# Kernel optimization log

Hardware: AMD Instinct MI355X
Metric: run time of the kernel (lower is better)

The kernel has to match this reference:

```python
import jax, jax.numpy as jnp
import numpy as np

P = 16
D = 768          # latent_dim
H = 3072         # hidden_dim
B = 256
OUT_DIMS = [100 + 10 * i for i in range(P)]   # sum = 2800
MAX_OUT = max(OUT_DIMS)
EPS = 1e-5


def setup_inputs() -> dict:
    key = jax.random.key(0)
    ks = jax.random.split(key, 6)
    x = jax.random.normal(ks[0], (B, P, D), dtype=jnp.float32)
    # LayerNorm params per part (torch default init: gamma=1, beta=0)
    gamma = jnp.ones((P, D), dtype=jnp.float32)
    beta = jnp.zeros((P, D), dtype=jnp.float32)
    # fc1: Linear(D, H, bias=False) per part -> stacked [P, H, D]
    w1 = jax.random.normal(ks[1], (P, H, D), dtype=jnp.float32) * 0.02
    # fc2: Linear(H, out_dims[i], bias=True) per part, padded to MAX_OUT.
    # Padded rows are never read (sliced away at concat).
    w2 = jax.random.normal(ks[2], (P, MAX_OUT, H), dtype=jnp.float32) * 0.02
    b2 = jnp.zeros((P, MAX_OUT), dtype=jnp.float32)
    return {"x": x, "gamma": gamma, "beta": beta, "w1": w1, "w2": w2, "b2": b2}


def reference(x, gamma, beta, w1, w2, b2):
    # Per-part LayerNorm over latent dim (torch uses biased variance)
    mu = jnp.mean(x, axis=-1, keepdims=True)
    var = jnp.mean(jnp.square(x - mu), axis=-1, keepdims=True)
    xn = (x - mu) * jax.lax.rsqrt(var + EPS) * gamma[None] + beta[None]  # [B,P,D]
    # fc1 (no bias) + exact GELU (torch.nn.GELU default)
    h = jnp.einsum('bpd,phd->bph', xn, w1)          # [B,P,H]
    h = jax.nn.gelu(h, approximate=False)
    # dropout p=0.0 -> identity
    # fc2 (with bias), padded grouped GEMM
    out_full = jnp.einsum('bph,poh->bpo', h, w2) + b2[None]  # [B,P,MAX_OUT]
    # concat variable-width slices along last dim
    out = jnp.concatenate([out_full[:, i, :OUT_DIMS[i]] for i in range(P)], axis=-1)
    return out  # [B, sum(OUT_DIMS)] = [256, 2800]
```

## Files before the change

### kernel.cpp

```cpp
#include <hip/hip_runtime.h>
#include <math.h>

typedef unsigned short u16;
typedef unsigned int u32;
typedef __attribute__((ext_vector_type(4))) float f32x4;
typedef __attribute__((ext_vector_type(8))) short bf16x8;

#define NP 16
#define DLAT 768
#define HDIM 3072
#define NB 256
#define MAXO 250
#define TOT 2800

__device__ __forceinline__ u16 f2b(float f) {
  union { float f; u32 u; } v; v.f = f;
  u32 u = v.u;
  u32 r = (u + 0x7fffu + ((u >> 16) & 1u)) >> 16;
  return (u16)r;
}

__device__ __forceinline__ u32 cvtpk(float lo, float hi) {
  u32 r;
  asm("v_cvt_pk_bf16_f32 %0, %1, %2" : "=v"(r) : "v"(lo), "v"(hi));
  return r;
}

__device__ __forceinline__ void gll16(const void* g, void* l) {
  __builtin_amdgcn_global_load_lds(
      (const __attribute__((address_space(1))) void*)g,
      (__attribute__((address_space(3))) void*)l, 16, 0, 0);
}

__global__ __launch_bounds__(256) void ln_kernel(
    const float* __restrict__ x, const float* __restrict__ gamma,
    const float* __restrict__ beta, u16* __restrict__ xn) {
  const int wave = threadIdx.x >> 6, lane = threadIdx.x & 63;
  const int row = blockIdx.x * 4 + wave;
  const int b = row >> 4, p = row & 15;
  const float4* xr = (const float4*)(x + (size_t)row * DLAT);
  const float4* g4 = (const float4*)(gamma + (size_t)p * DLAT);
  const float4* b4 = (const float4*)(beta + (size_t)p * DLAT);
  float4 v[3];
  float s = 0.f, ss = 0.f;
#pragma unroll
  for (int j = 0; j < 3; ++j) {
    v[j] = xr[lane + j * 64];
    s += v[j].x + v[j].y + v[j].z + v[j].w;
    ss += v[j].x * v[j].x + v[j].y * v[j].y + v[j].z * v[j].z + v[j].w * v[j].w;
  }
#pragma unroll
  for (int o = 32; o; o >>= 1) { s += __shfl_xor(s, o); ss += __shfl_xor(ss, o); }
  const float mu = s * (1.f / 768.f);
  const float var = ss * (1.f / 768.f) - mu * mu;
  const float rstd = rsqrtf(var + 1e-5f);
  u16* xo = xn + ((size_t)(p * NB + b)) * DLAT;
#pragma unroll
  for (int j = 0; j < 3; ++j) {
    const int f = lane + j * 64;
    float4 g = g4[f], be = b4[f];
    float o0 = (v[j].x - mu) * rstd * g.x + be.x;
    float o1 = (v[j].y - mu) * rstd * g.y + be.y;
    float o2 = (v[j].z - mu) * rstd * g.z + be.z;
    float o3 = (v[j].w - mu) * rstd * g.w + be.w;
    uint2 w;
    w.x = (u32)f2b(o0) | ((u32)f2b(o1) << 16);
    w.y = (u32)f2b(o2) | ((u32)f2b(o3) << 16);
    *(uint2*)&xo[f * 4] = w;
  }
}

__global__ __launch_bounds__(256) void fc1_kernel(
    const u16* __restrict__ xn, const float* __restrict__ w1, u16* __restrict__ h) {
  const int bid = blockIdx.x;
  const int xcd = bid & 7;
  const int j = bid >> 3;
  const int p = xcd * 2 + (j >= 48 ? 1 : 0);
  const int jj = j % 48;
  const int n0 = (jj >> 1) * 128;
  const int m0 = (jj & 1) * 128;

  const int tid = threadIdx.x;
  const int lane = tid & 63, wave = tid >> 6;
  const int lanelo = lane & 15, lanehi = lane >> 4;
  const int wr = wave >> 1, wc = wave & 1;

  const u16* Ap = xn + (size_t)p * NB * DLAT + (size_t)m0 * DLAT;
  const float* Bp = w1 + (size_t)p * HDIM * DLAT + (size_t)n0 * DLAT;

  __shared__ u16 As[2][128 * 32];
  __shared__ u16 Bs[2][128 * 32];

  int ag_src[2], ag_dst[2];
#pragma unroll
  for (int i = 0; i < 2; ++i) {
    const int s = wave * 64 + i * 256 + lane;
    const int r = s >> 2;
    const int g = (s & 3) ^ (r & 3);
    ag_src[i] = r * DLAT + g * 8;
    ag_dst[i] = (wave * 64 + i * 256) * 8;
  }
  const int rb = tid >> 1;
  const int kc = (tid & 1) * 16;
  const float* bg = Bp + (size_t)rb * DLAT + kc;
  int bw_off[2];
#pragma unroll
  for (int i = 0; i < 2; ++i) {
    const int g = (tid & 1) * 2 + i;
    bw_off[i] = (rb * 4 + (g ^ (rb & 3))) * 8;
  }
  int a_sl[4], b_sl[4];
#pragma unroll
  for (int m = 0; m < 4; ++m) {
    const int ra = wr * 64 + m * 16 + lanelo;
    a_sl[m] = (ra * 4 + (lanehi ^ (ra & 3))) * 8;
    const int rbl = wc * 64 + m * 16 + lanelo;
    b_sl[m] = (rbl * 4 + (lanehi ^ (rbl & 3))) * 8;
  }

  f32x4 acc[4][4] = {};
  float4 br[4];
  const int NK = DLAT / 32;

  auto issueA = [&](int kt) {
    const int k2 = kt * 32;
#pragma unroll
    for (int i = 0; i < 2; ++i)
      gll16(Ap + ag_src[i] + k2, &As[kt & 1][ag_dst[i]]);
  };
  auto loadB = [&](int kt) {
    const float* q = bg + kt * 32;
#pragma unroll
    for (int i = 0; i < 4; ++i) br[i] = *(const float4*)(q + i * 4);
  };
  auto writeB = [&](int kt) {
    u16* bb = &Bs[kt & 1][0];
    uint4 w0, w1v;
    w0.x = cvtpk(br[0].x, br[0].y); w0.y = cvtpk(br[0].z, br[0].w);
    w0.z = cvtpk(br[1].x, br[1].y); w0.w = cvtpk(br[1].z, br[1].w);
    w1v.x = cvtpk(br[2].x, br[2].y); w1v.y = cvtpk(br[2].z, br[2].w);
    w1v.z = cvtpk(br[3].x, br[3].y); w1v.w = cvtpk(br[3].z, br[3].w);
    *(uint4*)&bb[bw_off[0]] = w0;
    *(uint4*)&bb[bw_off[1]] = w1v;
  };

  issueA(0); loadB(0); writeB(0);
  __syncthreads();
#pragma unroll 2
  for (int kt = 0; kt < NK; ++kt) {
    const int cur = kt & 1;
    if (kt + 1 < NK) { issueA(kt + 1); loadB(kt + 1); }
    bf16x8 af[4], bf[4];
    const u16* a_ = &As[cur][0];
    const u16* b_ = &Bs[cur][0];
#pragma unroll
    for (int m = 0; m < 4; ++m) af[m] = *(const bf16x8*)&a_[a_sl[m]];
#pragma unroll
    for (int n = 0; n < 4; ++n) bf[n] = *(const bf16x8*)&b_[b_sl[n]];
#pragma unroll
    for (int m = 0; m < 4; ++m)
#pragma unroll
      for (int n = 0; n < 4; ++n)
        acc[m][n] = __builtin_amdgcn_mfma_f32_16x16x32_bf16(af[m], bf[n], acc[m][n], 0, 0, 0);
    if (kt + 1 < NK) writeB(kt + 1);
    __syncthreads();
  }

  u16* hp = h + (size_t)p * NB * HDIM;
#pragma unroll
  for (int m = 0; m < 4; ++m) {
#pragma unroll
    for (int n = 0; n < 4; ++n) {
      const int col = n0 + wc * 64 + n * 16 + lanelo;
#pragma unroll
      for (int r = 0; r < 4; ++r) {
        const int row = m0 + wr * 64 + m * 16 + lanehi * 4 + r;
        const float vv = acc[m][n][r];
        const float gel = 0.5f * vv * (1.f + erff(vv * 0.70710678118654752f));
        hp[(size_t)row * HDIM + col] = f2b(gel);
      }
    }
  }
}

__global__ __launch_bounds__(256) void fc2_kernel(
    const u16* __restrict__ hbuf, const float* __restrict__ w2,
    const float* __restrict__ b2, float* __restrict__ out) {
  const int bid = blockIdx.x;
  const int bs = (bid & 7) * 32 + (bid >> 3);
  const int p = bs >> 4;
  const int mb = (bs >> 2) & 3;
  const int nb = bs & 3;
  const int odim = 100 + 10 * p;
  const int n0 = nb * 64;
  if (n0 >= odim) return;
  const int m0 = mb * 64;
  const int off = 100 * p + 5 * p * (p - 1);

  const int tid = threadIdx.x;
  const int lane = tid & 63, wave = tid >> 6;
  const int lanelo = lane & 15, lanehi = lane >> 4;
  const int wr = wave >> 1, wc = wave & 1;

  const u16* Ap = hbuf + (size_t)p * NB * HDIM + (size_t)m0 * HDIM;
  const float* Bp = w2 + (size_t)p * MAXO * HDIM;

  __shared__ u16 As[3][64 * 32];
  __shared__ u16 Bs[2][64 * 32];

  int ag_off;
  const int ag_base = (64 * wave) * 8;
  {
    int slot = 64 * wave + lane;
    int r = slot >> 2;
    int c = (slot & 3) ^ ((r >> 1) & 3);
    ag_off = r * HDIM + c * 8;
  }
  const int br0 = min(n0 + (tid >> 3), MAXO - 1);
  const int br1 = min(n0 + (tid >> 3) + 32, MAXO - 1);
  const float* bg0 = Bp + (size_t)br0 * HDIM + (tid & 7) * 4;
  const float* bg1 = Bp + (size_t)br1 * HDIM + (tid & 7) * 4;
  int bso[2];
#pragma unroll
  for (int i = 0; i < 2; ++i) {
    int r = (tid >> 3) + 32 * i;
    int c = ((tid & 7) >> 1) ^ ((r >> 1) & 3);
    bso[i] = (r * 4 + c) * 8 + (tid & 1) * 4;
  }
  int a_sl[2], b_sl[2];
#pragma unroll
  for (int m = 0; m < 2; ++m) {
    int r = wr * 32 + m * 16 + lanelo;
    a_sl[m] = (r * 4 + (lanehi ^ ((r >> 1) & 3))) * 8;
    int rb = wc * 32 + m * 16 + lanelo;
    b_sl[m] = (rb * 4 + (lanehi ^ ((rb >> 1) & 3))) * 8;
  }

  f32x4 acc[2][2] = {};
  float4 bA0, bA1, bB0, bB1;
  const int NK = HDIM / 32;

  auto issue = [&](int kt, float4& r0, float4& r1) {
    const int k2 = kt * 32;
    gll16(Ap + ag_off + k2, &As[kt % 3][ag_base]);
    asm volatile("" ::: "memory");
    r0 = *(const float4*)(bg0 + k2);
    r1 = *(const float4*)(bg1 + k2);
    asm volatile("" ::: "memory");
  };

  auto step = [&](int kt, float4& r0, float4& r1) {
    if (kt + 1 < NK) asm volatile("s_waitcnt vmcnt(3)" ::: "memory");
    else             asm volatile("s_waitcnt vmcnt(0)" ::: "memory");
    {
      u16* bb = &Bs[kt & 1][0];
      uint2 w0, w1v;
      w0.x = (u32)f2b(r0.x) | ((u32)f2b(r0.y) << 16);
      w0.y = (u32)f2b(r0.z) | ((u32)f2b(r0.w) << 16);
      w1v.x = (u32)f2b(r1.x) | ((u32)f2b(r1.y) << 16);
      w1v.y = (u32)f2b(r1.z) | ((u32)f2b(r1.w) << 16);
      *(uint2*)&bb[bso[0]] = w0;
      *(uint2*)&bb[bso[1]] = w1v;
    }
    asm volatile("s_waitcnt lgkmcnt(0)" ::: "memory");
    __builtin_amdgcn_s_barrier();
    asm volatile("" ::: "memory");
    if (kt + 2 < NK) issue(kt + 2, r0, r1);
    const u16* a_ = &As[kt % 3][0];
    const u16* b_ = &Bs[kt & 1][0];
    bf16x8 af[2], bf[2];
#pragma unroll
    for (int m = 0; m < 2; ++m) af[m] = *(const bf16x8*)&a_[a_sl[m]];
#pragma unroll
    for (int n = 0; n < 2; ++n) bf[n] = *(const bf16x8*)&b_[b_sl[n]];
#pragma unroll
    for (int m = 0; m < 2; ++m)
#pragma unroll
      for (int n = 0; n < 2; ++n)
        acc[m][n] = __builtin_amdgcn_mfma_f32_16x16x32_bf16(af[m], bf[n], acc[m][n], 0, 0, 0);
  };

  issue(0, bA0, bA1);
  issue(1, bB0, bB1);
  for (int kt = 0; kt < NK; kt += 2) {
    step(kt, bA0, bA1);
    step(kt + 1, bB0, bB1);
  }

#pragma unroll
  for (int m = 0; m < 2; ++m) {
#pragma unroll
    for (int n = 0; n < 2; ++n) {
      const int col = n0 + wc * 32 + n * 16 + lanelo;
      if (col < odim) {
        const float bias = b2[(size_t)p * MAXO + col];
#pragma unroll
        for (int r = 0; r < 4; ++r) {
          const int row = m0 + wr * 32 + m * 16 + lanehi * 4 + r;
          out[(size_t)row * TOT + off + col] = acc[m][n][r] + bias;
        }
      }
    }
  }
}

extern "C" void kernel_launch(void* const* d_in, const int* in_sizes, int n_in,
                              void* d_out, int out_size, void* d_ws, size_t ws_size,
                              hipStream_t stream) {
  const float* x = (const float*)d_in[0];
  const float* gamma = (const float*)d_in[1];
  const float* beta = (const float*)d_in[2];
  const float* w1 = (const float*)d_in[3];
  const float* w2 = (const float*)d_in[4];
  const float* b2 = (const float*)d_in[5];
  float* out = (float*)d_out;

  u16* xn = (u16*)d_ws;
  u16* h = (u16*)d_ws + (size_t)NP * NB * DLAT;

  ln_kernel<<<1024, 256, 0, stream>>>(x, gamma, beta, xn);
  fc1_kernel<<<768, 256, 0, stream>>>(xn, w1, h);
  fc2_kernel<<<NP * 16, 256, 0, stream>>>(h, w2, b2, out);
}
```

Before: 102.7 us.

## Stream fp32 fc1 weights into LDS directly and convert to bf16 at fragment load

The fc1 kernel now loads the fp32 w1 tile straight into shared memory with direct global-to-LDS loads, instead of staging it through registers and converting before the LDS store. The bf16 conversion moves to the point where each MFMA fragment is read. The N tile shrinks from 128 to 64, which doubles the grid to 1536 blocks, and a launch-bounds occupancy hint is added. Block-to-part mapping and the LDS swizzles are reworked to match. This frees registers and overlaps weight loads asynchronously, at the cost of more LDS traffic, repeated conversions per M-wave, and less A-tile reuse.

```diff
diff --git a/kernel.cpp b/kernel.cpp
--- a/kernel.cpp
+++ b/kernel.cpp
@@ -70,15 +70,16 @@
   }
 }
 
-__global__ __launch_bounds__(256) void fc1_kernel(
+__global__ __launch_bounds__(256, 5) void fc1_kernel(
     const u16* __restrict__ xn, const float* __restrict__ w1, u16* __restrict__ h) {
   const int bid = blockIdx.x;
   const int xcd = bid & 7;
-  const int j = bid >> 3;
-  const int p = xcd * 2 + (j >= 48 ? 1 : 0);
-  const int jj = j % 48;
-  const int n0 = (jj >> 1) * 128;
-  const int m0 = (jj & 1) * 128;
+  const int q = bid >> 3;
+  const int g = xcd * 96 + (q >> 1);
+  const int mb = q & 1;
+  const int p = g / 48;
+  const int n0 = (g % 48) * 64;
+  const int m0 = mb * 128;
 
   const int tid = threadIdx.x;
   const int lane = tid & 63, wave = tid >> 6;
@@ -88,81 +89,80 @@
   const u16* Ap = xn + (size_t)p * NB * DLAT + (size_t)m0 * DLAT;
   const float* Bp = w1 + (size_t)p * HDIM * DLAT + (size_t)n0 * DLAT;
 
-  __shared__ u16 As[2][128 * 32];
-  __shared__ u16 Bs[2][128 * 32];
-
-  int ag_src[2], ag_dst[2];
+  __shared__ u16 AsU[2][128 * 32];
+  __shared__ float BsF[2][64 * 32];
+
+  int a_src[2], a_dst[2];
 #pragma unroll
   for (int i = 0; i < 2; ++i) {
-    const int s = wave * 64 + i * 256 + lane;
+    const int s = wave * 128 + i * 64 + lane;
     const int r = s >> 2;
-    const int g = (s & 3) ^ (r & 3);
-    ag_src[i] = r * DLAT + g * 8;
-    ag_dst[i] = (wave * 64 + i * 256) * 8;
-  }
-  const int rb = tid >> 1;
-  const int kc = (tid & 1) * 16;
-  const float* bg = Bp + (size_t)rb * DLAT + kc;
-  int bw_off[2];
+    const int gg = (s & 3) ^ ((r >> 1) & 3);
+    a_src[i] = r * DLAT + gg * 8;
+    a_dst[i] = (wave * 128 + i * 64) * 8;
+  }
+  int b_src[2], b_dst[2];
 #pragma unroll
   for (int i = 0; i < 2; ++i) {
-    const int g = (tid & 1) * 2 + i;
-    bw_off[i] = (rb * 4 + (g ^ (rb & 3))) * 8;
-  }
-  int a_sl[4], b_sl[4];
+    const int s = wave * 128 + i * 64 + lane;
+    const int r = s >> 3;
+    const int gg = (s & 7) ^ (r & 7);
+    b_src[i] = r * DLAT + gg * 4;
+    b_dst[i] = (wave * 128 + i * 64) * 4;
+  }
+  int a_sl[4];
 #pragma unroll
   for (int m = 0; m < 4; ++m) {
     const int ra = wr * 64 + m * 16 + lanelo;
-    a_sl[m] = (ra * 4 + (lanehi ^ (ra & 3))) * 8;
-    const int rbl = wc * 64 + m * 16 + lanelo;
-    b_sl[m] = (rbl * 4 + (lanehi ^ (rbl & 3))) * 8;
-  }
-
-  f32x4 acc[4][4] = {};
-  float4 br[4];
+    a_sl[m] = (ra * 4 + (lanehi ^ ((ra >> 1) & 3))) * 8;
+  }
+  int b_sl[2][2];
+#pragma unroll
+  for (int n = 0; n < 2; ++n) {
+    const int rbl = wc * 32 + n * 16 + lanelo;
+#pragma unroll
+    for (int jj = 0; jj < 2; ++jj)
+      b_sl[n][jj] = rbl * 32 + ((2 * lanehi + jj) ^ (rbl & 7)) * 4;
+  }
+
+  f32x4 acc[4][2] = {};
   const int NK = DLAT / 32;
 
-  auto issueA = [&](int kt) {
+  auto stage = [&](int kt) {
     const int k2 = kt * 32;
 #pragma unroll
     for (int i = 0; i < 2; ++i)
-      gll16(Ap + ag_src[i] + k2, &As[kt & 1][ag_dst[i]]);
+      gll16(Ap + a_src[i] + k2, &AsU[kt & 1][a_dst[i]]);
+#pragma unroll
+    for (int i = 0; i < 2; ++i)
+      gll16(Bp + b_src[i] + k2, &BsF[kt & 1][b_dst[i]]);
   };
-  auto loadB = [&](int kt) {
-    const float* q = bg + kt * 32;
-#pragma unroll
-    for (int i = 0; i < 4; ++i) br[i] = *(const float4*)(q + i * 4);
-  };
-  auto writeB = [&](int kt) {
-    u16* bb = &Bs[kt & 1][0];
-    uint4 w0, w1v;
-    w0.x = cvtpk(br[0].x, br[0].y); w0.y = cvtpk(br[0].z, br[0].w);
-    w0.z = cvtpk(br[1].x, br[1].y); w0.w = cvtpk(br[1].z, br[1].w);
-    w1v.x = cvtpk(br[2].x, br[2].y); w1v.y = cvtpk(br[2].z, br[2].w);
-    w1v.z = cvtpk(br[3].x, br[3].y); w1v.w = cvtpk(br[3].z, br[3].w);
-    *(uint4*)&bb[bw_off[0]] = w0;
-    *(uint4*)&bb[bw_off[1]] = w1v;
-  };
-
-  issueA(0); loadB(0); writeB(0);
+
+  stage(0);
   __syncthreads();
 #pragma unroll 2
   for (int kt = 0; kt < NK; ++kt) {
     const int cur = kt & 1;
-    if (kt + 1 < NK) { issueA(kt + 1); loadB(kt + 1); }
-    bf16x8 af[4], bf[4];
-    const u16* a_ = &As[cur][0];
-    const u16* b_ = &Bs[cur][0];
+    if (kt + 1 < NK) stage(kt + 1);
+    const u16* a_ = &AsU[cur][0];
+    const float* b_ = &BsF[cur][0];
+    bf16x8 af[4], bf[2];
 #pragma unroll
     for (int m = 0; m < 4; ++m) af[m] = *(const bf16x8*)&a_[a_sl[m]];
 #pragma unroll
-    for (int n = 0; n < 4; ++n) bf[n] = *(const bf16x8*)&b_[b_sl[n]];
+    for (int n = 0; n < 2; ++n) {
+      const float4 f0 = *(const float4*)&b_[b_sl[n][0]];
+      const float4 f1 = *(const float4*)&b_[b_sl[n][1]];
+      union { u32 u[4]; bf16x8 v; } t;
+      t.u[0] = cvtpk(f0.x, f0.y); t.u[1] = cvtpk(f0.z, f0.w);
+      t.u[2] = cvtpk(f1.x, f1.y); t.u[3] = cvtpk(f1.z, f1.w);
+      bf[n] = t.v;
+    }
 #pragma unroll
     for (int m = 0; m < 4; ++m)
 #pragma unroll
-      for (int n = 0; n < 4; ++n)
+      for (int n = 0; n < 2; ++n)
         acc[m][n] = __builtin_amdgcn_mfma_f32_16x16x32_bf16(af[m], bf[n], acc[m][n], 0, 0, 0);
-    if (kt + 1 < NK) writeB(kt + 1);
     __syncthreads();
   }
 
@@ -170,8 +170,8 @@
 #pragma unroll
   for (int m = 0; m < 4; ++m) {
 #pragma unroll
-    for (int n = 0; n < 4; ++n) {
-      const int col = n0 + wc * 64 + n * 16 + lanelo;
+    for (int n = 0; n < 2; ++n) {
+      const int col = n0 + wc * 32 + n * 16 + lanelo;
 #pragma unroll
       for (int r = 0; r < 4; ++r) {
         const int row = m0 + wr * 64 + m * 16 + lanehi * 4 + r;
@@ -319,6 +319,6 @@
   u16* h = (u16*)d_ws + (size_t)NP * NB * DLAT;
 
   ln_kernel<<<1024, 256, 0, stream>>>(x, gamma, beta, xn);
-  fc1_kernel<<<768, 256, 0, stream>>>(xn, w1, h);
+  fc1_kernel<<<1536, 256, 0, stream>>>(xn, w1, h);
   fc2_kernel<<<NP * 16, 256, 0, stream>>>(h, w2, b2, out);
 }
```

Result: slower. 106.5 us (+3.6%).

## Load fp32 W1 tiles to LDS directly and convert to bf16 at fragment read

Applied to the files above, without the earlier changes.

The fc1 kernel no longer loads W1 into registers, converts it to bf16 and writes that to LDS. Both A and B tiles now go straight to LDS with direct global-to-LDS loads over a 64-wide K chunk, and W1 stays fp32 in LDS until it is converted during fragment reads. Each block also starts its K loop at a different chunk offset to spread memory traffic. The intent is to cut register-staging and VALU work in the load path, at the cost of a single-buffered LDS that no longer overlaps loads with MFMA, twice the LDS footprint for B, and repeated conversions.

```diff
diff --git a/kernel.cpp b/kernel.cpp
--- a/kernel.cpp
+++ b/kernel.cpp
@@ -88,81 +88,59 @@
   const u16* Ap = xn + (size_t)p * NB * DLAT + (size_t)m0 * DLAT;
   const float* Bp = w1 + (size_t)p * HDIM * DLAT + (size_t)n0 * DLAT;
 
-  __shared__ u16 As[2][128 * 32];
-  __shared__ u16 Bs[2][128 * 32];
-
-  int ag_src[2], ag_dst[2];
-#pragma unroll
-  for (int i = 0; i < 2; ++i) {
-    const int s = wave * 64 + i * 256 + lane;
-    const int r = s >> 2;
-    const int g = (s & 3) ^ (r & 3);
-    ag_src[i] = r * DLAT + g * 8;
-    ag_dst[i] = (wave * 64 + i * 256) * 8;
-  }
-  const int rb = tid >> 1;
-  const int kc = (tid & 1) * 16;
-  const float* bg = Bp + (size_t)rb * DLAT + kc;
-  int bw_off[2];
-#pragma unroll
-  for (int i = 0; i < 2; ++i) {
-    const int g = (tid & 1) * 2 + i;
-    bw_off[i] = (rb * 4 + (g ^ (rb & 3))) * 8;
-  }
-  int a_sl[4], b_sl[4];
-#pragma unroll
-  for (int m = 0; m < 4; ++m) {
-    const int ra = wr * 64 + m * 16 + lanelo;
-    a_sl[m] = (ra * 4 + (lanehi ^ (ra & 3))) * 8;
-    const int rbl = wc * 64 + m * 16 + lanelo;
-    b_sl[m] = (rbl * 4 + (lanehi ^ (rbl & 3))) * 8;
+  __shared__ u16 As[128 * 64];
+  __shared__ float Bs[128 * 64];
+
+  int a_src[4], b_src[8];
+#pragma unroll
+  for (int jx = 0; jx < 4; ++jx) {
+    const int s = tid + 256 * jx, r = s >> 3, c = s & 7;
+    a_src[jx] = r * DLAT + ((c ^ (r & 7)) << 3);
+  }
+#pragma unroll
+  for (int jx = 0; jx < 8; ++jx) {
+    const int s = tid + 256 * jx, r = s >> 4, c = s & 15;
+    b_src[jx] = r * DLAT + ((c ^ (r & 7)) << 2);
   }
 
   f32x4 acc[4][4] = {};
-  float4 br[4];
-  const int NK = DLAT / 32;
-
-  auto issueA = [&](int kt) {
-    const int k2 = kt * 32;
-#pragma unroll
-    for (int i = 0; i < 2; ++i)
-      gll16(Ap + ag_src[i] + k2, &As[kt & 1][ag_dst[i]]);
-  };
-  auto loadB = [&](int kt) {
-    const float* q = bg + kt * 32;
-#pragma unroll
-    for (int i = 0; i < 4; ++i) br[i] = *(const float4*)(q + i * 4);
-  };
-  auto writeB = [&](int kt) {
-    u16* bb = &Bs[kt & 1][0];
-    uint4 w0, w1v;
-    w0.x = cvtpk(br[0].x, br[0].y); w0.y = cvtpk(br[0].z, br[0].w);
-    w0.z = cvtpk(br[1].x, br[1].y); w0.w = cvtpk(br[1].z, br[1].w);
-    w1v.x = cvtpk(br[2].x, br[2].y); w1v.y = cvtpk(br[2].z, br[2].w);
-    w1v.z = cvtpk(br[3].x, br[3].y); w1v.w = cvtpk(br[3].z, br[3].w);
-    *(uint4*)&bb[bw_off[0]] = w0;
-    *(uint4*)&bb[bw_off[1]] = w1v;
-  };
-
-  issueA(0); loadB(0); writeB(0);
-  __syncthreads();
-#pragma unroll 2
-  for (int kt = 0; kt < NK; ++kt) {
-    const int cur = kt & 1;
-    if (kt + 1 < NK) { issueA(kt + 1); loadB(kt + 1); }
-    bf16x8 af[4], bf[4];
-    const u16* a_ = &As[cur][0];
-    const u16* b_ = &Bs[cur][0];
-#pragma unroll
-    for (int m = 0; m < 4; ++m) af[m] = *(const bf16x8*)&a_[a_sl[m]];
-#pragma unroll
-    for (int n = 0; n < 4; ++n) bf[n] = *(const bf16x8*)&b_[b_sl[n]];
-#pragma unroll
-    for (int m = 0; m < 4; ++m)
-#pragma unroll
-      for (int n = 0; n < 4; ++n)
-        acc[m][n] = __builtin_amdgcn_mfma_f32_16x16x32_bf16(af[m], bf[n], acc[m][n], 0, 0, 0);
-    if (kt + 1 < NK) writeB(kt + 1);
+  const int st = bid % 12;
+
+  for (int cc = 0; cc < 12; ++cc) {
+    const int ch = (cc + st) % 12;
+    const int k2 = ch * 64;
+#pragma unroll
+    for (int jx = 0; jx < 4; ++jx)
+      gll16(Ap + a_src[jx] + k2, &As[(tid + 256 * jx) * 8]);
+#pragma unroll
+    for (int jx = 0; jx < 8; ++jx)
+      gll16(Bp + b_src[jx] + k2, &Bs[(tid + 256 * jx) * 4]);
+    __syncthreads();
+#pragma unroll
+    for (int kt = 0; kt < 2; ++kt) {
+      bf16x8 af[4], bf[4];
+#pragma unroll
+      for (int m = 0; m < 4; ++m) {
+        const int ra = wr * 64 + m * 16 + lanelo;
+        af[m] = *(const bf16x8*)&As[ra * 64 + (((kt * 4 + lanehi) ^ (ra & 7)) << 3)];
+      }
+#pragma unroll
+      for (int n = 0; n < 4; ++n) {
+        const int rb = wc * 64 + n * 16 + lanelo;
+        const int c0 = kt * 8 + lanehi * 2;
+        const float4 f0 = *(const float4*)&Bs[rb * 64 + ((c0 ^ (rb & 7)) << 2)];
+        const float4 f1 = *(const float4*)&Bs[rb * 64 + (((c0 + 1) ^ (rb & 7)) << 2)];
+        union { u32 u[4]; bf16x8 v; } t;
+        t.u[0] = cvtpk(f0.x, f0.y); t.u[1] = cvtpk(f0.z, f0.w);
+        t.u[2] = cvtpk(f1.x, f1.y); t.u[3] = cvtpk(f1.z, f1.w);
+        bf[n] = t.v;
+      }
+#pragma unroll
+      for (int m = 0; m < 4; ++m)
+#pragma unroll
+        for (int n = 0; n < 4; ++n)
+          acc[m][n] = __builtin_amdgcn_mfma_f32_16x16x32_bf16(af[m], bf[n], acc[m][n], 0, 0, 0);
+    }
     __syncthreads();
   }
 
```

Measured after the change: 119.1 us. +16.0%, slower.
